# Kernel tuning notes

Measured on AMD Instinct MI355X. Metric: run time of the kernel, lower is better.

Reference implementation:

```python
import jax, jax.numpy as jnp
import numpy as np

N_NODES = 100000
N_EDGES = 600000
H = 128          # hidden_units
LH = 256         # lin_hidden_units
F_IN = 3         # num_features (x, y, area)
C = 8            # out_classes


def setup_inputs() -> dict:
    key = jax.random.key(0)
    ks = jax.random.split(key, 12)
    s = 0.05
    return {
        "x": jax.random.normal(ks[0], (N_NODES, F_IN), dtype=jnp.float32),
        "edge_index": jax.random.randint(ks[1], (2, N_EDGES), 0, N_NODES, dtype=jnp.int64),
        # conv1: lin_l (aggregated neighbors, has bias), lin_r (root, no bias)
        "Wl1": jax.random.normal(ks[2], (H, F_IN), dtype=jnp.float32) * s,
        "bl1": jnp.zeros((H,), dtype=jnp.float32),
        "Wr1": jax.random.normal(ks[3], (H, F_IN), dtype=jnp.float32) * s,
        # conv2
        "Wl2": jax.random.normal(ks[4], (H, H), dtype=jnp.float32) * s,
        "bl2": jnp.zeros((H,), dtype=jnp.float32),
        "Wr2": jax.random.normal(ks[5], (H, H), dtype=jnp.float32) * s,
        # MLP head
        "W1": jax.random.normal(ks[6], (LH, H), dtype=jnp.float32) * s,
        "b1": jnp.zeros((LH,), dtype=jnp.float32),
        "W2": jax.random.normal(ks[7], (C, LH), dtype=jnp.float32) * s,
        "b2": jnp.zeros((C,), dtype=jnp.float32),
    }


def _normalize(x):
    coords = x[:, :2]                      # [N, 2]
    areas = x[:, 2:3]                      # [N, 1]
    mx = jnp.max(coords, axis=0)
    mn = jnp.min(coords, axis=0)
    theta = jnp.float32(np.pi / 2)
    c, sn = jnp.cos(theta), jnp.sin(theta)
    R = jnp.array([[1.0, 0.0], [0.0, 1.0]], dtype=x.dtype) * c + \
        jnp.array([[0.0, -1.0], [1.0, 0.0]], dtype=x.dtype) * sn
    rotated = coords @ R.T                 # (R @ coords.T).T
    rotate = (mx[1] - mn[1]) > (mx[0] - mn[0])
    coords = jnp.where(rotate, rotated, coords)
    coords = (coords - jnp.mean(coords, axis=0)) / jnp.max(coords, axis=0)
    areas = areas / jnp.max(areas, axis=0)
    return jnp.concatenate([coords, areas], axis=-1)


def _sage_conv(x, src, dst, Wl, bl, Wr):
    # mean aggregation of source features at target nodes
    msg = x[src]                                               # [E, d] gather
    agg = jax.ops.segment_sum(msg, dst, num_segments=N_NODES)  # [N, d]
    deg = jax.ops.segment_sum(jnp.ones((src.shape[0],), x.dtype), dst,
                              num_segments=N_NODES)
    agg = agg / jnp.maximum(deg, 1.0)[:, None]
    return agg @ Wl.T + bl + x @ Wr.T


def reference(x, edge_index, Wl1, bl1, Wr1, Wl2, bl2, Wr2, W1, b1, W2, b2):
    src, dst = edge_index[0], edge_index[1]
    h = _normalize(x)
    h = jnp.tanh(_sage_conv(h, src, dst, Wl1, bl1, Wr1))
    h = jnp.tanh(_sage_conv(h, src, dst, Wl2, bl2, Wr2))
    h = jnp.tanh(h @ W1.T + b1)
    h = h @ W2.T + b2
    return jax.nn.softmax(h, axis=1)
```

## Files before the change

### kernel.cpp

```cpp
#include <hip/hip_runtime.h>
#include <hip/hip_bf16.h>
#include <math.h>

#define N_NODES 100000
#define N_EDGES 600000
#define H 128
#define LH 256
#define CDIM 8
#define NB_STATS 256
#define NT128 ((N_NODES + 127) / 128)
#define ELLW 64
#define NB_NODE ((N_NODES + 255) / 256)

#define NBUCK 391
#define NBLK_P1 256
#define EPB ((N_EDGES + NBLK_P1 - 1) / NBLK_P1)
#define CAP 26

typedef __attribute__((ext_vector_type(8))) short short8;
typedef __attribute__((ext_vector_type(4))) float floatx4;

#define OFF_PART   0
#define OFF_DEG    2816
#define OFF_H0     (OFF_DEG + N_NODES)
#define OFF_ELL    (OFF_H0 + N_NODES*4)
#define OFF_CNTT   (OFF_ELL + N_NODES*ELLW)
#define OFF_SCR    (OFF_CNTT + NBUCK*NBLK_P1)
#define OFF_WPK2   (OFF_SCR + NBUCK*NBLK_P1*CAP*2)
#define OFF_WPK1   (OFF_WPK2 + 16384)
#define OFF_W2PK   (OFF_WPK1 + 16384)
#define OFF_XB     (OFF_W2PK + 2048)

__device__ __forceinline__ float rot_c() { return cosf(1.57079632679489661923f); }
__device__ __forceinline__ float rot_s() { return sinf(1.57079632679489661923f); }
__device__ __forceinline__ float bfhi(unsigned v) { return __uint_as_float(v & 0xffff0000u); }
__device__ __forceinline__ float bflo(unsigned v) { return __uint_as_float(v << 16); }
__device__ __forceinline__ unsigned short bfu(float f) {
    __hip_bfloat16 h = __float2bfloat16(f);
    return *(unsigned short*)&h;
}
__device__ __forceinline__ float ftanh(float x) {
    float e = __expf(2.0f * x);
    return 1.0f - 2.0f * __builtin_amdgcn_rcpf(e + 1.0f);
}

__global__ __launch_bounds__(256) void statsPart_k(const float* __restrict__ x,
        float* __restrict__ part, const int* __restrict__ ei,
        int* __restrict__ cntT, int2* __restrict__ scratch) {
    __shared__ float red[4][11];
    __shared__ int lcnt[NBUCK];
    int tid = threadIdx.x;

    if (blockIdx.x >= NB_STATS) {
        int blk = blockIdx.x - NB_STATS;
        for (int i = tid; i < NBUCK; i += 256) lcnt[i] = 0;
        __syncthreads();
        int base = blk * EPB;
        int lim = base + EPB;
        if (lim > N_EDGES) lim = N_EDGES;
        for (int e = base + tid; e < lim; e += 256) {
            int s = ei[e], d = ei[N_EDGES + e];
            int b = d >> 8;
            int pos = atomicAdd(&lcnt[b], 1);
            scratch[(b * NBLK_P1 + blk) * CAP + pos] = make_int2(s, d);
        }
        __syncthreads();
        for (int i = tid; i < NBUCK; i += 256)
            cntT[i * NBLK_P1 + blk] = lcnt[i];
        return;
    }

    const float c = rot_c(), sn = rot_s();
    float mn0 = INFINITY, mx0 = -INFINITY, mn1 = INFINITY, mx1 = -INFINITY;
    float s0 = 0.f, s1 = 0.f, sr0 = 0.f, sr1 = 0.f;
    float mxr0 = -INFINITY, mxr1 = -INFINITY, mxa = -INFINITY;
    for (int i = blockIdx.x * 256 + tid; i < N_NODES; i += NB_STATS * 256) {
        float x0 = x[3*i], x1 = x[3*i+1], a = x[3*i+2];
        float r0 = c*x0 - sn*x1;
        float r1 = sn*x0 + c*x1;
        mn0 = fminf(mn0, x0); mx0 = fmaxf(mx0, x0);
        mn1 = fminf(mn1, x1); mx1 = fmaxf(mx1, x1);
        s0 += x0; s1 += x1; sr0 += r0; sr1 += r1;
        mxr0 = fmaxf(mxr0, r0); mxr1 = fmaxf(mxr1, r1);
        mxa = fmaxf(mxa, a);
    }
    float vals[11] = {mn0, mx0, mn1, mx1, s0, s1, sr0, sr1, mxr0, mxr1, mxa};
    int lane = tid & 63, wave = tid >> 6;
    #pragma unroll
    for (int v = 0; v < 11; v++) {
        const int op = (v==0||v==2) ? 0 : (v>=4 && v<=7) ? 2 : 1;
        float val = vals[v];
        #pragma unroll
        for (int off = 32; off > 0; off >>= 1) {
            float o = __shfl_down(val, off);
            val = (op==0) ? fminf(val,o) : (op==1) ? fmaxf(val,o) : (val+o);
        }
        if (lane == 0) red[wave][v] = val;
    }
    __syncthreads();
    if (tid < 11) {
        int v = tid;
        int op = (v==0||v==2) ? 0 : (v>=4 && v<=7) ? 2 : 1;
        float a = red[0][v], b = red[1][v], cc = red[2][v], d = red[3][v];
        float r = (op==0) ? fminf(fminf(a,b), fminf(cc,d))
                : (op==1) ? fmaxf(fmaxf(a,b), fmaxf(cc,d))
                : (a + b + cc + d);
        part[blockIdx.x * 11 + v] = r;
    }
}

__global__ __launch_bounds__(256) void binNorm_k(const float* __restrict__ x,
        const float* __restrict__ part, float4* __restrict__ h0,
        const float* __restrict__ Wl2, const float* __restrict__ Wr2,
        const float* __restrict__ W1, const float* __restrict__ W2,
        __hip_bfloat16* __restrict__ Wpk2, __hip_bfloat16* __restrict__ Wpk1,
        __hip_bfloat16* __restrict__ W2pk,
        const int* __restrict__ cntT, const int2* __restrict__ scratch,
        int* __restrict__ ell, int* __restrict__ deg) {
    __shared__ int pref[NBLK_P1 + 1];
    __shared__ int scn[NBLK_P1];
    __shared__ int ncnt[256];
    __shared__ float res[11];
    int tid = threadIdx.x;

    if (blockIdx.x < NBUCK) {
        int b = blockIdx.x;
        ncnt[tid] = 0;
        scn[tid] = cntT[b * NBLK_P1 + tid];
        __syncthreads();
        for (int off = 1; off < NBLK_P1; off <<= 1) {
            int v = (tid >= off) ? scn[tid - off] : 0;
            __syncthreads();
            scn[tid] += v;
            __syncthreads();
        }
        if (tid == 0) pref[0] = 0;
        pref[tid + 1] = scn[tid];
        __syncthreads();
        int T = pref[NBLK_P1];
        for (int f = tid; f < T; f += 256) {
            int lo = 0, hi = NBLK_P1;
            while (hi - lo > 1) {
                int mid = (lo + hi) >> 1;
                if (pref[mid] <= f) lo = mid; else hi = mid;
            }
            int2 sd = scratch[(b * NBLK_P1 + lo) * CAP + (f - pref[lo])];
            int pos = atomicAdd(&ncnt[sd.y & 255], 1);
            ell[(sd.y << 6) + pos] = sd.x;
        }
        __syncthreads();
        int n = (b << 8) + tid;
        if (n < N_NODES) deg[n] = ncnt[tid];
        return;
    }

    int nb = blockIdx.x - NBUCK;
    int i = nb * 256 + tid;
    if (tid < 64) {
        const int ops[11] = {0,1,0,1,2,2,2,2,1,1,1};
        for (int v = 0; v < 11; v++) {
            float val = part[tid * 11 + v];
            #pragma unroll
            for (int p = 1; p < 4; p++) {
                float o = part[(tid + p*64) * 11 + v];
                val = (ops[v]==0) ? fminf(val,o) : (ops[v]==1) ? fmaxf(val,o) : (val+o);
            }
            #pragma unroll
            for (int off = 32; off > 0; off >>= 1) {
                float o = __shfl_down(val, off);
                val = (ops[v]==0) ? fminf(val,o) : (ops[v]==1) ? fmaxf(val,o) : (val+o);
            }
            if (tid == 0) res[v] = val;
        }
    }
    __syncthreads();
    int rotate = (res[3] - res[2]) > (res[1] - res[0]);
    float mean0 = (rotate ? res[6] : res[4]) / (float)N_NODES;
    float mean1 = (rotate ? res[7] : res[5]) / (float)N_NODES;
    float imx0  = 1.0f / (rotate ? res[8] : res[1]);
    float imx1  = 1.0f / (rotate ? res[9] : res[3]);
    float imxa  = 1.0f / res[10];

    if (i < N_NODES) {
        const float c = rot_c(), sn = rot_s();
        float x0 = x[3*i], x1 = x[3*i+1], a = x[3*i+2];
        float u0 = rotate ? (c*x0 - sn*x1) : x0;
        float u1 = rotate ? (sn*x0 + c*x1) : x1;
        h0[i] = make_float4((u0 - mean0) * imx0, (u1 - mean1) * imx1, a * imxa, 0.f);
    }
    int idx = i;
    if (idx < 32768) {
        int j = idx & 7, lane = (idx >> 3) & 63, nt = (idx >> 9) & 7, ks = idx >> 12;
        int k = ks*32 + (lane >> 4)*8 + j;
        int n = nt*16 + (lane & 15);
        float v = (k < 128) ? Wl2[n*H + k] : Wr2[n*H + (k - 128)];
        Wpk2[idx] = __float2bfloat16(v);
    } else if (idx < 65536) {
        int i2 = idx - 32768;
        int j = i2 & 7, lane = (i2 >> 3) & 63, nt = (i2 >> 9) & 15, ks = i2 >> 13;
        int k = ks*32 + (lane >> 4)*8 + j;
        int n = nt*16 + (lane & 15);
        Wpk1[i2] = __float2bfloat16(W1[n*H + k]);
    } else if (idx < 69632) {
        int i3 = idx - 65536;
        int j = i3 & 7, lane = (i3 >> 3) & 63, ks = i3 >> 9;
        int k = ks*32 + (lane >> 4)*8 + j;
        int n = lane & 15;
        W2pk[i3] = __float2bfloat16((n < CDIM) ? W2[n*LH + k] : 0.f);
    }
}

__global__ __launch_bounds__(256) void agg1conv1_k(const float4* __restrict__ h0,
        const int* __restrict__ deg, const int* __restrict__ ell,
        const float* __restrict__ Wl1, const float* __restrict__ bl1,
        const float* __restrict__ Wr1, __hip_bfloat16* __restrict__ Xb) {
    __shared__ float wl[H*3], wr[H*3], bb[H];
    __shared__ float4 sa[256];
    int tid = threadIdx.x;
    for (int i = tid; i < H*3; i += 256) { wl[i] = Wl1[i]; wr[i] = Wr1[i]; }
    if (tid < H) bb[tid] = bl1[tid];
    int base = blockIdx.x * 256;
    int n = base + tid;
    float4 av = make_float4(0.f, 0.f, 0.f, 0.f);
    if (n < N_NODES) {
        int dg = deg[n];
        int start = n << 6, end = start + dg;
        float a0 = 0.f, a1 = 0.f, a2 = 0.f;
        int e = start;
        for (; e + 3 < end; e += 4) {
            int s0 = ell[e], s1 = ell[e+1], s2 = ell[e+2], s3 = ell[e+3];
            float4 v0 = h0[s0];
            float4 v1 = h0[s1];
            float4 v2 = h0[s2];
            float4 v3 = h0[s3];
            a0 += (v0.x + v1.x) + (v2.x + v3.x);
            a1 += (v0.y + v1.y) + (v2.y + v3.y);
            a2 += (v0.z + v1.z) + (v2.z + v3.z);
        }
        for (; e < end; e++) {
            float4 v = h0[ell[e]];
            a0 += v.x; a1 += v.y; a2 += v.z;
        }
        float inv = 1.0f / (float)max(dg, 1);
        av = make_float4(a0 * inv, a1 * inv, a2 * inv, 0.f);
    }
    sa[tid] = av;
    __syncthreads();
    int sub = tid >> 6;
    int j2 = (tid & 63) * 2;
    for (int i = 0; i < 64; i++) {
        int loc = i * 4 + sub;
        int nn = base + loc;
        if (nn >= N_NODES) break;
        float4 a = sa[loc];
        float4 xv = h0[nn];
        float o0 = wl[3*j2+0]*a.x + wl[3*j2+1]*a.y + wl[3*j2+2]*a.z + bb[j2]
                 + wr[3*j2+0]*xv.x + wr[3*j2+1]*xv.y + wr[3*j2+2]*xv.z;
        float o1 = wl[3*j2+3]*a.x + wl[3*j2+4]*a.y + wl[3*j2+5]*a.z + bb[j2+1]
                 + wr[3*j2+3]*xv.x + wr[3*j2+4]*xv.y + wr[3*j2+5]*xv.z;
        unsigned pv = ((unsigned)bfu(ftanh(o1)) << 16) | (unsigned)bfu(ftanh(o0));
        *(unsigned*)&Xb[(size_t)nn*256 + 128 + j2] = pv;
    }
}

__global__ void agg2_k(__hip_bfloat16* __restrict__ Xb, const int* __restrict__ deg,
                       const int* __restrict__ ell) {
    int lane = threadIdx.x & 15;
    int n = blockIdx.x * 16 + (threadIdx.x >> 4);
    int dg = deg[n];
    int start = n << 6, end = start + dg;
    const short* XbS = (const short*)Xb;
    float a0=0.f,a1=0.f,a2=0.f,a3=0.f,a4=0.f,a5=0.f,a6=0.f,a7=0.f;
    int e = start;
    for (; e + 3 < end; e += 4) {
        int s0 = ell[e], s1 = ell[e+1], s2 = ell[e+2], s3 = ell[e+3];
        uint4 v0 = *(const uint4*)&XbS[(size_t)s0*256 + 128 + lane*8];
        uint4 v1 = *(const uint4*)&XbS[(size_t)s1*256 + 128 + lane*8];
        uint4 v2 = *(const uint4*)&XbS[(size_t)s2*256 + 128 + lane*8];
        uint4 v3 = *(const uint4*)&XbS[(size_t)s3*256 + 128 + lane*8];
        a0 += (bflo(v0.x) + bflo(v1.x)) + (bflo(v2.x) + bflo(v3.x));
        a1 += (bfhi(v0.x) + bfhi(v1.x)) + (bfhi(v2.x) + bfhi(v3.x));
        a2 += (bflo(v0.y) + bflo(v1.y)) + (bflo(v2.y) + bflo(v3.y));
        a3 += (bfhi(v0.y) + bfhi(v1.y)) + (bfhi(v2.y) + bfhi(v3.y));
        a4 += (bflo(v0.z) + bflo(v1.z)) + (bflo(v2.z) + bflo(v3.z));
        a5 += (bfhi(v0.z) + bfhi(v1.z)) + (bfhi(v2.z) + bfhi(v3.z));
        a6 += (bflo(v0.w) + bflo(v1.w)) + (bflo(v2.w) + bflo(v3.w));
        a7 += (bfhi(v0.w) + bfhi(v1.w)) + (bfhi(v2.w) + bfhi(v3.w));
    }
    for (; e < end; e++) {
        int s0 = ell[e];
        uint4 v0 = *(const uint4*)&XbS[(size_t)s0*256 + 128 + lane*8];
        a0 += bflo(v0.x); a1 += bfhi(v0.x);
        a2 += bflo(v0.y); a3 += bfhi(v0.y);
        a4 += bflo(v0.z); a5 += bfhi(v0.z);
        a6 += bflo(v0.w); a7 += bfhi(v0.w);
    }
    float inv = 1.0f / (float)max(dg, 1);
    uint4 o;
    o.x = ((unsigned)bfu(a1*inv) << 16) | (unsigned)bfu(a0*inv);
    o.y = ((unsigned)bfu(a3*inv) << 16) | (unsigned)bfu(a2*inv);
    o.z = ((unsigned)bfu(a5*inv) << 16) | (unsigned)bfu(a4*inv);
    o.w = ((unsigned)bfu(a7*inv) << 16) | (unsigned)bfu(a6*inv);
    *(uint4*)&Xb[(size_t)n*256 + lane*8] = o;
}

__global__ __launch_bounds__(512, 1) void conv2mlp_k(const __hip_bfloat16* __restrict__ Xb,
        const __hip_bfloat16* __restrict__ Wpk2, const float* __restrict__ bl2,
        const __hip_bfloat16* __restrict__ Wpk1, const float* __restrict__ b1,
        const __hip_bfloat16* __restrict__ W2pk, const float* __restrict__ b2,
        float* __restrict__ out) {
    __shared__ short Ws2[32768];
    __shared__ short Ws1[32768];
    __shared__ short Cs[8 * 16 * 128];
    int tid = threadIdx.x;
    int lane = tid & 63, wave = tid >> 6;
    int quad = lane >> 4, m = lane & 15, c0 = lane & 15;
    {
        const float4* s2 = (const float4*)Wpk2;
        const float4* s1 = (const float4*)Wpk1;
        float4* d2 = (float4*)Ws2;
        float4* d1 = (float4*)Ws1;
        #pragma unroll
        for (int i = 0; i < 8; i++) {
            d2[tid + i*512] = s2[tid + i*512];
            d1[tid + i*512] = s1[tid + i*512];
        }
    }
    short8 w2f[8];
    #pragma unroll
    for (int ks = 0; ks < 8; ks++)
        w2f[ks] = *(const short8*)&W2pk[(ks*64 + lane)*8];
    float bl2r[8], b1r[16];
    #pragma unroll
    for (int nt = 0; nt < 8; nt++) bl2r[nt] = bl2[nt*16 + c0];
    #pragma unroll
    for (int nt = 0; nt < 16; nt++) b1r[nt] = b1[nt*16 + c0];
    float b2v = (c0 < CDIM) ? b2[c0] : 0.f;
    __syncthreads();
    short* Tw = &Cs[wave * (16 * 128)];

    int tile = blockIdx.x;
    short8 areg[8];
    {
        int row = tile*128 + wave*16 + m;
        int rowL = row < N_NODES ? row : N_NODES - 1;
        const short* Arow = (const short*)Xb + (size_t)rowL * 256;
        #pragma unroll
        for (int ks = 0; ks < 8; ks++)
            areg[ks] = *(const short8*)(Arow + ks*32 + quad*8);
    }
    for (; tile < NT128; tile += gridDim.x) {
        short8 anext[8];
        {
            int tnext = tile + gridDim.x;
            int rown = (tnext < NT128) ? (tnext*128 + wave*16 + m) : 0;
            int rowNL = rown < N_NODES ? rown : N_NODES - 1;
            const short* ArowN = (const short*)Xb + (size_t)rowNL * 256;
            #pragma unroll
            for (int ks = 0; ks < 8; ks++)
                anext[ks] = *(const short8*)(ArowN + ks*32 + quad*8);
        }
        floatx4 acc2[8];
        #pragma unroll
        for (int i = 0; i < 8; i++)
            #pragma unroll
            for (int r = 0; r < 4; r++) acc2[i][r] = 0.f;
        #pragma unroll
        for (int ks = 0; ks < 8; ks++) {
            #pragma unroll
            for (int nt = 0; nt < 8; nt++) {
                short8 b = *(const short8*)&Ws2[((ks*8 + nt)*64 + lane)*8];
                acc2[nt] = __builtin_amdgcn_mfma_f32_16x16x32_bf16(areg[ks], b, acc2[nt], 0, 0, 0);
            }
        }
        #pragma unroll
        for (int nt = 0; nt < 8; nt++) {
            int cg = nt*2 + (c0 >> 3);
            #pragma unroll
            for (int r = 0; r < 4; r++) {
                int row = quad*4 + r;
                Tw[row*128 + ((cg ^ row) << 3) + (c0 & 7)] =
                    (short)bfu(ftanh(acc2[nt][r] + bl2r[nt]));
            }
        }
        floatx4 acc1[16];
        #pragma unroll
        for (int i = 0; i < 16; i++)
            #pragma unroll
            for (int r = 0; r < 4; r++) acc1[i][r] = 0.f;
        #pragma unroll
        for (int ks = 0; ks < 4; ks++) {
            short8 a = *(const short8*)&Tw[m*128 + (((ks*4 + quad) ^ m) << 3)];
            #pragma unroll
            for (int nt = 0; nt < 16; nt++) {
                short8 b = *(const short8*)&Ws1[((ks*16 + nt)*64 + lane)*8];
                acc1[nt] = __builtin_amdgcn_mfma_f32_16x16x32_bf16(a, b, acc1[nt], 0, 0, 0);
            }
        }
        floatx4 lacc;
        #pragma unroll
        for (int r = 0; r < 4; r++) lacc[r] = 0.f;
        #pragma unroll
        for (int ch = 0; ch < 4; ch++) {
            #pragma unroll
            for (int ntl = 0; ntl < 4; ntl++) {
                int nt = ch*4 + ntl;
                int cg = ntl*2 + (c0 >> 3);
                #pragma unroll
                for (int r = 0; r < 4; r++) {
                    int row = quad*4 + r;
                    Tw[row*128 + ((cg ^ row) << 3) + (c0 & 7)] =
                        (short)bfu(ftanh(acc1[nt][r] + b1r[nt]));
                }
            }
            #pragma unroll
            for (int k2 = 0; k2 < 2; k2++) {
                short8 a = *(const short8*)&Tw[m*128 + (((k2*4 + quad) ^ m) << 3)];
                lacc = __builtin_amdgcn_mfma_f32_16x16x32_bf16(a, w2f[ch*2 + k2], lacc, 0, 0, 0);
            }
        }
        int rbase = tile*128 + wave*16 + quad*4;
        #pragma unroll
        for (int r = 0; r < 4; r++) {
            float v = lacc[r] + b2v;
            float mval = (c0 < CDIM) ? v : -INFINITY;
            #pragma unroll
            for (int off = 1; off < 8; off <<= 1)
                mval = fmaxf(mval, __shfl_xor(mval, off));
            float e = (c0 < CDIM) ? __expf(v - mval) : 0.f;
            float ssum = e;
            #pragma unroll
            for (int off = 1; off < 8; off <<= 1)
                ssum += __shfl_xor(ssum, off);
            int rowg = rbase + r;
            if (c0 < CDIM && rowg < N_NODES)
                out[(size_t)rowg*CDIM + c0] = e / ssum;
        }
        #pragma unroll
        for (int ks = 0; ks < 8; ks++) areg[ks] = anext[ks];
    }
}

extern "C" void kernel_launch(void* const* d_in, const int* in_sizes, int n_in,
                              void* d_out, int out_size, void* d_ws, size_t ws_size,
                              hipStream_t stream) {
    const float* x   = (const float*)d_in[0];
    const int*   ei  = (const int*)d_in[1];
    const float* Wl1 = (const float*)d_in[2];
    const float* bl1 = (const float*)d_in[3];
    const float* Wr1 = (const float*)d_in[4];
    const float* Wl2 = (const float*)d_in[5];
    const float* bl2 = (const float*)d_in[6];
    const float* Wr2 = (const float*)d_in[7];
    const float* W1  = (const float*)d_in[8];
    const float* b1  = (const float*)d_in[9];
    const float* W2  = (const float*)d_in[10];
    const float* b2  = (const float*)d_in[11];

    float* ws     = (float*)d_ws;
    float* part   = ws + OFF_PART;
    int*   deg    = (int*)(ws + OFF_DEG);
    float4* h0    = (float4*)(ws + OFF_H0);
    int*   ell    = (int*)(ws + OFF_ELL);
    int*   cntT   = (int*)(ws + OFF_CNTT);
    int2*  scratch= (int2*)(ws + OFF_SCR);
    __hip_bfloat16* Wpk2 = (__hip_bfloat16*)(ws + OFF_WPK2);
    __hip_bfloat16* Wpk1 = (__hip_bfloat16*)(ws + OFF_WPK1);
    __hip_bfloat16* W2pk = (__hip_bfloat16*)(ws + OFF_W2PK);
    __hip_bfloat16* Xb   = (__hip_bfloat16*)(ws + OFF_XB);

    statsPart_k<<<NB_STATS + NBLK_P1, 256, 0, stream>>>(x, part, ei, cntT, scratch);
    binNorm_k<<<NBUCK + NB_NODE, 256, 0, stream>>>(x, part, h0,
            Wl2, Wr2, W1, W2, Wpk2, Wpk1, W2pk, cntT, scratch, ell, deg);
    agg1conv1_k<<<NB_NODE, 256, 0, stream>>>(h0, deg, ell,
            Wl1, bl1, Wr1, Xb);
    agg2_k<<<N_NODES / 16, 256, 0, stream>>>(Xb, deg, ell);
    conv2mlp_k<<<256, 512, 0, stream>>>(Xb, Wpk2, bl2, Wpk1, b1, W2pk, b2,
            (float*)d_out);
}
```

Before: 196.3 us.

## Process two 16-row groups per wave in fused MLP head kernel

The final fused conv2-linear/MLP/softmax kernel now handles 256-row tiles, with each wave computing two 16-row MFMA groups that share each Ws2 B-fragment load from LDS. The layer-1 and layer-2 stages then run per row group through the wave's LDS scratch. The software prefetch of the next tile's A rows is removed, so global loads are no longer overlapped with compute. Register pressure rises from the doubled A registers and accumulators, which may lower occupancy, and the larger tile halves the tile count, which may hurt load balance.

Result: no change. 197.2 us (+0.5%).

```diff
diff --git a/kernel.cpp b/kernel.cpp
--- a/kernel.cpp
+++ b/kernel.cpp
@@ -8,7 +8,7 @@
 #define LH 256
 #define CDIM 8
 #define NB_STATS 256
-#define NT128 ((N_NODES + 127) / 128)
+#define NT256 ((N_NODES + 255) / 256)
 #define ELLW 64
 #define NB_NODE ((N_NODES + 255) / 256)
 
@@ -339,105 +339,101 @@
     __syncthreads();
     short* Tw = &Cs[wave * (16 * 128)];
 
-    int tile = blockIdx.x;
-    short8 areg[8];
-    {
-        int row = tile*128 + wave*16 + m;
-        int rowL = row < N_NODES ? row : N_NODES - 1;
-        const short* Arow = (const short*)Xb + (size_t)rowL * 256;
-        #pragma unroll
-        for (int ks = 0; ks < 8; ks++)
-            areg[ks] = *(const short8*)(Arow + ks*32 + quad*8);
-    }
-    for (; tile < NT128; tile += gridDim.x) {
-        short8 anext[8];
-        {
-            int tnext = tile + gridDim.x;
-            int rown = (tnext < NT128) ? (tnext*128 + wave*16 + m) : 0;
-            int rowNL = rown < N_NODES ? rown : N_NODES - 1;
-            const short* ArowN = (const short*)Xb + (size_t)rowNL * 256;
-            #pragma unroll
-            for (int ks = 0; ks < 8; ks++)
-                anext[ks] = *(const short8*)(ArowN + ks*32 + quad*8);
-        }
-        floatx4 acc2[8];
-        #pragma unroll
-        for (int i = 0; i < 8; i++)
-            #pragma unroll
-            for (int r = 0; r < 4; r++) acc2[i][r] = 0.f;
+    for (int tile = blockIdx.x; tile < NT256; tile += gridDim.x) {
+        int row0 = tile*256 + wave*32 + m;
+        int row1 = row0 + 16;
+        int r0L = row0 < N_NODES ? row0 : N_NODES - 1;
+        int r1L = row1 < N_NODES ? row1 : N_NODES - 1;
+        const short* Arow0 = (const short*)Xb + (size_t)r0L * 256;
+        const short* Arow1 = (const short*)Xb + (size_t)r1L * 256;
+        short8 areg0[8], areg1[8];
+        #pragma unroll
+        for (int ks = 0; ks < 8; ks++) {
+            areg0[ks] = *(const short8*)(Arow0 + ks*32 + quad*8);
+            areg1[ks] = *(const short8*)(Arow1 + ks*32 + quad*8);
+        }
+        floatx4 acc2[2][8];
+        #pragma unroll
+        for (int g = 0; g < 2; g++)
+            #pragma unroll
+            for (int i = 0; i < 8; i++)
+                #pragma unroll
+                for (int r = 0; r < 4; r++) acc2[g][i][r] = 0.f;
         #pragma unroll
         for (int ks = 0; ks < 8; ks++) {
             #pragma unroll
             for (int nt = 0; nt < 8; nt++) {
                 short8 b = *(const short8*)&Ws2[((ks*8 + nt)*64 + lane)*8];
-                acc2[nt] = __builtin_amdgcn_mfma_f32_16x16x32_bf16(areg[ks], b, acc2[nt], 0, 0, 0);
-            }
-        }
-        #pragma unroll
-        for (int nt = 0; nt < 8; nt++) {
-            int cg = nt*2 + (c0 >> 3);
+                acc2[0][nt] = __builtin_amdgcn_mfma_f32_16x16x32_bf16(areg0[ks], b, acc2[0][nt], 0, 0, 0);
+                acc2[1][nt] = __builtin_amdgcn_mfma_f32_16x16x32_bf16(areg1[ks], b, acc2[1][nt], 0, 0, 0);
+            }
+        }
+        #pragma unroll
+        for (int rg = 0; rg < 2; rg++) {
+            #pragma unroll
+            for (int nt = 0; nt < 8; nt++) {
+                int cg = nt*2 + (c0 >> 3);
+                #pragma unroll
+                for (int r = 0; r < 4; r++) {
+                    int rw = quad*4 + r;
+                    Tw[rw*128 + ((cg ^ rw) << 3) + (c0 & 7)] =
+                        (short)bfu(ftanh(acc2[rg][nt][r] + bl2r[nt]));
+                }
+            }
+            floatx4 acc1[16];
+            #pragma unroll
+            for (int i = 0; i < 16; i++)
+                #pragma unroll
+                for (int r = 0; r < 4; r++) acc1[i][r] = 0.f;
+            #pragma unroll
+            for (int ks = 0; ks < 4; ks++) {
+                short8 a = *(const short8*)&Tw[m*128 + (((ks*4 + quad) ^ m) << 3)];
+                #pragma unroll
+                for (int nt = 0; nt < 16; nt++) {
+                    short8 b = *(const short8*)&Ws1[((ks*16 + nt)*64 + lane)*8];
+                    acc1[nt] = __builtin_amdgcn_mfma_f32_16x16x32_bf16(a, b, acc1[nt], 0, 0, 0);
+                }
+            }
+            floatx4 lacc;
+            #pragma unroll
+            for (int r = 0; r < 4; r++) lacc[r] = 0.f;
+            #pragma unroll
+            for (int ch = 0; ch < 4; ch++) {
+                #pragma unroll
+                for (int ntl = 0; ntl < 4; ntl++) {
+                    int nt = ch*4 + ntl;
+                    int cg = ntl*2 + (c0 >> 3);
+                    #pragma unroll
+                    for (int r = 0; r < 4; r++) {
+                        int rw = quad*4 + r;
+                        Tw[rw*128 + ((cg ^ rw) << 3) + (c0 & 7)] =
+                            (short)bfu(ftanh(acc1[nt][r] + b1r[nt]));
+                    }
+                }
+                #pragma unroll
+                for (int k2 = 0; k2 < 2; k2++) {
+                    short8 a = *(const short8*)&Tw[m*128 + (((k2*4 + quad) ^ m) << 3)];
+                    lacc = __builtin_amdgcn_mfma_f32_16x16x32_bf16(a, w2f[ch*2 + k2], lacc, 0, 0, 0);
+                }
+            }
+            int rbase = tile*256 + wave*32 + rg*16 + quad*4;
             #pragma unroll
             for (int r = 0; r < 4; r++) {
-                int row = quad*4 + r;
-                Tw[row*128 + ((cg ^ row) << 3) + (c0 & 7)] =
-                    (short)bfu(ftanh(acc2[nt][r] + bl2r[nt]));
-            }
-        }
-        floatx4 acc1[16];
-        #pragma unroll
-        for (int i = 0; i < 16; i++)
-            #pragma unroll
-            for (int r = 0; r < 4; r++) acc1[i][r] = 0.f;
-        #pragma unroll
-        for (int ks = 0; ks < 4; ks++) {
-            short8 a = *(const short8*)&Tw[m*128 + (((ks*4 + quad) ^ m) << 3)];
-            #pragma unroll
-            for (int nt = 0; nt < 16; nt++) {
-                short8 b = *(const short8*)&Ws1[((ks*16 + nt)*64 + lane)*8];
-                acc1[nt] = __builtin_amdgcn_mfma_f32_16x16x32_bf16(a, b, acc1[nt], 0, 0, 0);
-            }
-        }
-        floatx4 lacc;
-        #pragma unroll
-        for (int r = 0; r < 4; r++) lacc[r] = 0.f;
-        #pragma unroll
-        for (int ch = 0; ch < 4; ch++) {
-            #pragma unroll
-            for (int ntl = 0; ntl < 4; ntl++) {
-                int nt = ch*4 + ntl;
-                int cg = ntl*2 + (c0 >> 3);
-                #pragma unroll
-                for (int r = 0; r < 4; r++) {
-                    int row = quad*4 + r;
-                    Tw[row*128 + ((cg ^ row) << 3) + (c0 & 7)] =
-                        (short)bfu(ftanh(acc1[nt][r] + b1r[nt]));
-                }
-            }
-            #pragma unroll
-            for (int k2 = 0; k2 < 2; k2++) {
-                short8 a = *(const short8*)&Tw[m*128 + (((k2*4 + quad) ^ m) << 3)];
-                lacc = __builtin_amdgcn_mfma_f32_16x16x32_bf16(a, w2f[ch*2 + k2], lacc, 0, 0, 0);
-            }
-        }
-        int rbase = tile*128 + wave*16 + quad*4;
-        #pragma unroll
-        for (int r = 0; r < 4; r++) {
-            float v = lacc[r] + b2v;
-            float mval = (c0 < CDIM) ? v : -INFINITY;
-            #pragma unroll
-            for (int off = 1; off < 8; off <<= 1)
-                mval = fmaxf(mval, __shfl_xor(mval, off));
-            float e = (c0 < CDIM) ? __expf(v - mval) : 0.f;
-            float ssum = e;
-            #pragma unroll
-            for (int off = 1; off < 8; off <<= 1)
-                ssum += __shfl_xor(ssum, off);
-            int rowg = rbase + r;
-            if (c0 < CDIM && rowg < N_NODES)
-                out[(size_t)rowg*CDIM + c0] = e / ssum;
-        }
-        #pragma unroll
-        for (int ks = 0; ks < 8; ks++) areg[ks] = anext[ks];
+                float v = lacc[r] + b2v;
+                float mval = (c0 < CDIM) ? v : -INFINITY;
+                #pragma unroll
+                for (int off = 1; off < 8; off <<= 1)
+                    mval = fmaxf(mval, __shfl_xor(mval, off));
+                float e = (c0 < CDIM) ? __expf(v - mval) : 0.f;
+                float ssum = e;
+                #pragma unroll
+                for (int off = 1; off < 8; off <<= 1)
+                    ssum += __shfl_xor(ssum, off);
+                int rowg = rbase + r;
+                if (c0 < CDIM && rowg < N_NODES)
+                    out[(size_t)rowg*CDIM + c0] = e / ssum;
+            }
+        }
     }
 }
 
```
